# Kernel tuning notes

Measured on AMD Instinct MI355X. Metric: run time of the kernel, lower is better.

## Reference

```python
import jax, jax.numpy as jnp
import numpy as np

N_EMBD = 768
N_HEAD = 8
B, T = 4, 2048

def setup_inputs() -> dict:
    key = jax.random.key(0)
    k1, k2, k3, k4, k5 = jax.random.split(key, 5)
    C = N_EMBD
    s = 1.0 / np.sqrt(C)
    return {
        "x": jax.random.normal(k1, (B, T, C), dtype=jnp.float32),
        "W_attn": jax.random.normal(k2, (C, 3 * C), dtype=jnp.float32) * s,
        "b_attn": jnp.zeros((3 * C,), dtype=jnp.float32),
        "W_proj": jax.random.normal(k3, (C, C), dtype=jnp.float32) * s,
        "b_proj": jnp.zeros((C,), dtype=jnp.float32),
    }

def reference(x, W_attn, b_attn, W_proj, b_proj):
    Bs, Ts, C = x.shape
    H = N_HEAD
    hs = C // H
    qkv = x @ W_attn + b_attn                      # [B,T,3C]
    q, k, v = jnp.split(qkv, 3, axis=-1)
    # reshape to [B,H,T,hs]
    q = q.reshape(Bs, Ts, H, hs).transpose(0, 2, 1, 3)
    k = k.reshape(Bs, Ts, H, hs).transpose(0, 2, 1, 3)
    v = v.reshape(Bs, Ts, H, hs).transpose(0, 2, 1, 3)
    scale = 1.0 / jnp.sqrt(jnp.float32(hs))
    att = jnp.einsum('bhid,bhjd->bhij', q, k) * scale   # [B,H,T,T]
    mask = jnp.tril(jnp.ones((Ts, Ts), dtype=bool))
    att = jnp.where(mask, att, -jnp.inf)
    m = jnp.max(att, axis=-1, keepdims=True)
    e = jnp.where(mask, jnp.exp(att - m), 0.0)
    # original kernel divides by (sum + 1e-9)
    att = e / (jnp.sum(e, axis=-1, keepdims=True) + 1e-9)
    y = jnp.einsum('bhij,bhjd->bhid', att, v)           # [B,H,T,hs]
    y = y.transpose(0, 2, 1, 3).reshape(Bs, Ts, C)
    return y @ W_proj + b_proj
```

## Files before the change

kernel.cpp:

```cpp
#include <hip/hip_runtime.h>

typedef __bf16 bf16;
typedef __attribute__((ext_vector_type(4))) __bf16 bf16x4;
typedef __attribute__((ext_vector_type(8))) __bf16 bf16x8;
typedef __attribute__((ext_vector_type(4))) float f32x4;

#define B_   4
#define T_   2048
#define C_   768
#define H_   8
#define HS_  96
#define M_   (B_ * T_)
#define QKN_ (3 * C_)

#define NEG_BIG (-1e30f)

#define KSTR 104
#define VSTR 72
#define PSTR 72

__device__ __forceinline__ void gload_lds16(const bf16* g, bf16* l) {
    __builtin_amdgcn_global_load_lds(
        (const __attribute__((address_space(1))) uint32_t*)g,
        (__attribute__((address_space(3))) uint32_t*)l,
        16, 0, 0);
}

__global__ void transpose_kernel(const float* __restrict__ W, bf16* __restrict__ Wt,
                                 int R, int Cn) {
    __shared__ bf16 tile[32][33];
    int tx = threadIdx.x, ty = threadIdx.y;
    int x  = blockIdx.x * 32 + tx;
    int y0 = blockIdx.y * 32;
#pragma unroll
    for (int j = 0; j < 32; j += 8)
        tile[ty + j][tx] = (bf16)W[(size_t)(y0 + ty + j) * Cn + x];
    __syncthreads();
    int y2 = blockIdx.x * 32;
    int x2 = y0 + tx;
#pragma unroll
    for (int j = 0; j < 32; j += 8)
        Wt[(size_t)(y2 + ty + j) * R + x2] = tile[tx][ty + j];
}

__global__ void sentinel_kernel(float* __restrict__ out, int n) {
    int i = blockIdx.x * 256 + threadIdx.x;
    if (i < n) out[i] = 12345.0f;
}

__device__ __forceinline__ bf16x8 cvt8(f32x4 v0, f32x4 v1) {
    bf16x8 o;
#pragma unroll
    for (int i = 0; i < 4; ++i) { o[i] = (bf16)v0[i]; o[4 + i] = (bf16)v1[i]; }
    return o;
}

__global__ __launch_bounds__(256) void convert_bf16_kernel(const float* __restrict__ in,
                                                           bf16* __restrict__ out,
                                                           int n8) {
    int i = blockIdx.x * 256 + threadIdx.x;
    if (i >= n8) return;
    const float* p = in + (size_t)i * 8;
    f32x4 a = *(const f32x4*)p;
    f32x4 b = *(const f32x4*)(p + 4);
    *(bf16x8*)&out[(size_t)i * 8] = cvt8(a, b);
}

#define TILE_ELEMS (128 * 64)

__global__ __launch_bounds__(256) void gemm_qkv(const bf16* __restrict__ A,
                                                const bf16* __restrict__ Bt,
                                                const float* __restrict__ bias,
                                                bf16* __restrict__ Cmat,
                                                bf16* __restrict__ Vt,
                                                int M, int N, int K) {
    __shared__ bf16 lda[2 * TILE_ELEMS];
    __shared__ bf16 ldb[2 * TILE_ELEMS];
    int tid  = threadIdx.x;
    int w    = tid >> 6;
    int lane = tid & 63;
    int col  = lane & 15, quad = lane >> 4;
    int wr   = w >> 1, wc = w & 1;
    int m0   = blockIdx.y * 128, n0 = blockIdx.x * 128;

    int srow = lane >> 3;
    int scol = (lane & 7) * 8;
    const bf16* gA[4]; const bf16* gB[4]; bf16* lA[4]; bf16* lB[4];
#pragma unroll
    for (int i = 0; i < 4; ++i) {
        int seg = w * 4 + i;
        int row = seg * 8 + srow;
        gA[i] = &A[(size_t)(m0 + row) * K + scol];
        gB[i] = &Bt[(size_t)(n0 + row) * K + scol];
        lA[i] = &lda[seg * 512];
        lB[i] = &ldb[seg * 512];
    }

    const f32x4 zero = {0.f, 0.f, 0.f, 0.f};
    f32x4 acc[4][4];
#pragma unroll
    for (int mr = 0; mr < 4; ++mr)
#pragma unroll
        for (int nc = 0; nc < 4; ++nc) acc[mr][nc] = zero;

#pragma unroll
    for (int i = 0; i < 4; ++i) {
        gload_lds16(gA[i], lA[i]);
        gload_lds16(gB[i], lB[i]);
    }
    __syncthreads();

    int cur = 0;
    for (int k0 = 0; k0 < K; k0 += 64) {
        int nxt = cur ^ 1;
        if (k0 + 64 < K) {
#pragma unroll
            for (int i = 0; i < 4; ++i) {
                gload_lds16(gA[i] + k0 + 64, lA[i] + nxt * TILE_ELEMS);
                gload_lds16(gB[i] + k0 + 64, lB[i] + nxt * TILE_ELEMS);
            }
        }
        const bf16* la = &lda[cur * TILE_ELEMS];
        const bf16* lb = &ldb[cur * TILE_ELEMS];
#pragma unroll
        for (int ks = 0; ks < 2; ++ks) {
            bf16x8 af[4], bfr[4];
#pragma unroll
            for (int t = 0; t < 4; ++t) {
                af[t]  = *(const bf16x8*)&la[(wr * 64 + t * 16 + col) * 64 + ks * 32 + quad * 8];
                bfr[t] = *(const bf16x8*)&lb[(wc * 64 + t * 16 + col) * 64 + ks * 32 + quad * 8];
            }
#pragma unroll
            for (int mr = 0; mr < 4; ++mr)
#pragma unroll
                for (int nc = 0; nc < 4; ++nc)
                    acc[mr][nc] = __builtin_amdgcn_mfma_f32_16x16x32_bf16(
                        af[mr], bfr[nc], acc[mr][nc], 0, 0, 0);
        }
        __syncthreads();
        cur = nxt;
    }

#pragma unroll
    for (int nc = 0; nc < 4; ++nc) {
        int n = n0 + wc * 64 + nc * 16 + col;
        float bv = bias[n];
#pragma unroll
        for (int mr = 0; mr < 4; ++mr) {
#pragma unroll
            for (int r = 0; r < 4; ++r) {
                int row = m0 + wr * 64 + mr * 16 + quad * 4 + r;
                Cmat[(size_t)row * N + n] = (bf16)(acc[mr][nc][r] + bv);
            }
        }
    }
    if (n0 >= 2 * C_) {
        int batch = m0 >> 11;
        bf16* Vtb = Vt + (size_t)batch * C_ * T_;
        int t0 = (m0 & 2047) + wr * 64;
#pragma unroll
        for (int nc = 0; nc < 4; ++nc) {
            int n  = n0 + wc * 64 + nc * 16 + col;
            int vc = n - 2 * C_;
            float bv = bias[n];
#pragma unroll
            for (int mr = 0; mr < 4; ++mr) {
                int t = t0 + mr * 16 + quad * 4;
                bf16x4 pk = {(bf16)(acc[mr][nc][0] + bv), (bf16)(acc[mr][nc][1] + bv),
                             (bf16)(acc[mr][nc][2] + bv), (bf16)(acc[mr][nc][3] + bv)};
                *(bf16x4*)&Vtb[(size_t)vc * T_ + t] = pk;
            }
        }
    }
}

__global__ __launch_bounds__(256) void gemm_proj(const bf16* __restrict__ A,
                                                 const bf16* __restrict__ Bt,
                                                 const float* __restrict__ bias,
                                                 float* __restrict__ Cmat,
                                                 int M, int N, int K) {
    __shared__ bf16 lda[2 * TILE_ELEMS];
    __shared__ bf16 ldb[2 * TILE_ELEMS];
    int tid  = threadIdx.x;
    int w    = tid >> 6;
    int lane = tid & 63;
    int col  = lane & 15, quad = lane >> 4;
    int wr   = w >> 1, wc = w & 1;
    int m0   = blockIdx.y * 128, n0 = blockIdx.x * 128;

    int srow = lane >> 3;
    int scol = (lane & 7) * 8;
    const bf16* gA[4]; const bf16* gB[4]; bf16* lA[4]; bf16* lB[4];
#pragma unroll
    for (int i = 0; i < 4; ++i) {
        int seg = w * 4 + i;
        int row = seg * 8 + srow;
        gA[i] = &A[(size_t)(m0 + row) * K + scol];
        gB[i] = &Bt[(size_t)(n0 + row) * K + scol];
        lA[i] = &lda[seg * 512];
        lB[i] = &ldb[seg * 512];
    }

    const f32x4 zero = {0.f, 0.f, 0.f, 0.f};
    f32x4 acc[4][4];
#pragma unroll
    for (int mr = 0; mr < 4; ++mr)
#pragma unroll
        for (int nc = 0; nc < 4; ++nc) acc[mr][nc] = zero;

#pragma unroll
    for (int i = 0; i < 4; ++i) {
        gload_lds16(gA[i], lA[i]);
        gload_lds16(gB[i], lB[i]);
    }
    __syncthreads();

    int cur = 0;
    for (int k0 = 0; k0 < K; k0 += 64) {
        int nxt = cur ^ 1;
        if (k0 + 64 < K) {
#pragma unroll
            for (int i = 0; i < 4; ++i) {
                gload_lds16(gA[i] + k0 + 64, lA[i] + nxt * TILE_ELEMS);
                gload_lds16(gB[i] + k0 + 64, lB[i] + nxt * TILE_ELEMS);
            }
        }
        const bf16* la = &lda[cur * TILE_ELEMS];
        const bf16* lb = &ldb[cur * TILE_ELEMS];
#pragma unroll
        for (int ks = 0; ks < 2; ++ks) {
            bf16x8 af[4], bfr[4];
#pragma unroll
            for (int t = 0; t < 4; ++t) {
                af[t]  = *(const bf16x8*)&la[(wr * 64 + t * 16 + col) * 64 + ks * 32 + quad * 8];
                bfr[t] = *(const bf16x8*)&lb[(wc * 64 + t * 16 + col) * 64 + ks * 32 + quad * 8];
            }
#pragma unroll
            for (int mr = 0; mr < 4; ++mr)
#pragma unroll
                for (int nc = 0; nc < 4; ++nc)
                    acc[mr][nc] = __builtin_amdgcn_mfma_f32_16x16x32_bf16(
                        af[mr], bfr[nc], acc[mr][nc], 0, 0, 0);
        }
        __syncthreads();
        cur = nxt;
    }

#pragma unroll
    for (int nc = 0; nc < 4; ++nc) {
        int n = n0 + wc * 64 + nc * 16 + col;
        float bv = bias[n];
#pragma unroll
        for (int mr = 0; mr < 4; ++mr) {
#pragma unroll
            for (int r = 0; r < 4; ++r) {
                int row = m0 + wr * 64 + mr * 16 + quad * 4 + r;
                Cmat[(size_t)row * N + n] = acc[mr][nc][r] + bv;
            }
        }
    }
}

__global__ __launch_bounds__(256) void attn_kernel(const bf16* __restrict__ qkv,
                                                   const bf16* __restrict__ Vt,
                                                   bf16* __restrict__ y,
                                                   int nGroups) {
    __shared__ bf16 ldsK[64 * KSTR];
    __shared__ bf16 ldsV[96 * VSTR];
    __shared__ bf16 ldsP[4 * 16 * PSTR];
    const int bid  = blockIdx.x;
    const int qt   = 31 - bid / nGroups;
    const int g    = bid % nGroups;
    const int h    = g & 7, b = g >> 3;
    const int tid  = threadIdx.x;
    const int w    = tid >> 6, lane = tid & 63;
    const int col  = lane & 15, quad = lane >> 4;
    const float SCALE2 = 0.10206207261596577f * 1.4426950408889634f;
    const float M0 = 24.0f;
    const f32x4 zero = {0.f, 0.f, 0.f, 0.f};

    const bf16* qkvb = qkv + (size_t)b * T_ * QKN_;
    const bf16* Vtbh = Vt + (size_t)(b * H_ + h) * HS_ * T_;
    bf16* yb  = y + (size_t)b * T_ * C_;
    bf16* myP = &ldsP[w * 16 * PSTR];

    const int rbase = qt * 64 + w * 16;

    bf16x8 qf[3];
#pragma unroll
    for (int c = 0; c < 3; ++c)
        qf[c] = *(const bf16x8*)&qkvb[(size_t)(rbase + col) * QKN_ + h * HS_ + c * 32 + quad * 8];

    const bf16* pK[3]; const bf16* pV[3];
    bf16 *dK[3], *dV[3];
#pragma unroll
    for (int i = 0; i < 3; ++i) {
        int chunk = i * 256 + tid;
        int rK = chunk / 12, cK = chunk - rK * 12;
        pK[i] = qkvb + (size_t)rK * QKN_ + C_ + h * HS_ + cK * 8;
        dK[i] = &ldsK[rK * KSTR + cK * 8];
        int rV = chunk >> 3, cV = chunk & 7;
        pV[i] = Vtbh + (size_t)rV * T_ + cV * 8;
        dV[i] = &ldsV[rV * VSTR + cV * 8];
    }

    f32x4 o[6];
#pragma unroll
    for (int n2 = 0; n2 < 6; ++n2) o[n2] = zero;
    float lsum = 0.f;

    bf16x8 kreg[3], vreg[3];
#pragma unroll
    for (int i = 0; i < 3; ++i) {
        kreg[i] = *(const bf16x8*)pK[i];
        vreg[i] = *(const bf16x8*)pV[i];
        pK[i] += (size_t)64 * QKN_;
        pV[i] += 64;
    }

    const int njt = qt + 1;
    for (int jt = 0; jt < njt; ++jt) {
        int jb = jt * 64;
        __syncthreads();
#pragma unroll
        for (int i = 0; i < 3; ++i) {
            *(bf16x8*)dK[i] = kreg[i];
            *(bf16x8*)dV[i] = vreg[i];
        }
        __syncthreads();
        if (jt + 1 < njt) {
#pragma unroll
            for (int i = 0; i < 3; ++i) {
                kreg[i] = *(const bf16x8*)pK[i];
                vreg[i] = *(const bf16x8*)pV[i];
                pK[i] += (size_t)64 * QKN_;
                pV[i] += 64;
            }
        }

        bf16x8 kf[4][3];
#pragma unroll
        for (int nb = 0; nb < 4; ++nb)
#pragma unroll
            for (int c = 0; c < 3; ++c)
                kf[nb][c] = *(const bf16x8*)&ldsK[(nb * 16 + col) * KSTR + c * 32 + quad * 8];

        f32x4 st[4];
#pragma unroll
        for (int nb = 0; nb < 4; ++nb) st[nb] = zero;
#pragma unroll
        for (int c = 0; c < 3; ++c)
#pragma unroll
            for (int nb = 0; nb < 4; ++nb)
                st[nb] = __builtin_amdgcn_mfma_f32_16x16x32_bf16(
                    kf[nb][c], qf[c], st[nb], 0, 0, 0);

        if (jt == njt - 1) {
#pragma unroll
            for (int nb = 0; nb < 4; ++nb)
#pragma unroll
                for (int r = 0; r < 4; ++r) {
                    int jg = jb + nb * 16 + quad * 4 + r;
                    st[nb][r] = (jg <= rbase + col) ? fmaf(st[nb][r], SCALE2, -M0)
                                                    : NEG_BIG;
                }
        } else {
#pragma unroll
            for (int nb = 0; nb < 4; ++nb)
#pragma unroll
                for (int r = 0; r < 4; ++r)
                    st[nb][r] = fmaf(st[nb][r], SCALE2, -M0);
        }

#pragma unroll
        for (int nb = 0; nb < 4; ++nb) {
#pragma unroll
            for (int r = 0; r < 4; ++r) {
                float pv = exp2f(st[nb][r]);
                st[nb][r] = pv;
                lsum += pv;
            }
            bf16x4 pk = {(bf16)st[nb][0], (bf16)st[nb][1],
                         (bf16)st[nb][2], (bf16)st[nb][3]};
            *(bf16x4*)&myP[col * PSTR + nb * 16 + quad * 4] = pk;
        }

        bf16x8 vf[6][2];
#pragma unroll
        for (int n2 = 0; n2 < 6; ++n2)
#pragma unroll
            for (int c = 0; c < 2; ++c)
                vf[n2][c] = *(const bf16x8*)&ldsV[(n2 * 16 + col) * VSTR + c * 32 + quad * 8];
        bf16x8 pa0 = *(const bf16x8*)&myP[col * PSTR + quad * 8];
        bf16x8 pa1 = *(const bf16x8*)&myP[col * PSTR + 32 + quad * 8];
#pragma unroll
        for (int n2 = 0; n2 < 6; ++n2)
            o[n2] = __builtin_amdgcn_mfma_f32_16x16x32_bf16(vf[n2][0], pa0, o[n2], 0, 0, 0);
#pragma unroll
        for (int n2 = 0; n2 < 6; ++n2)
            o[n2] = __builtin_amdgcn_mfma_f32_16x16x32_bf16(vf[n2][1], pa1, o[n2], 0, 0, 0);
    }

    lsum += __shfl_xor(lsum, 16, 64);
    lsum += __shfl_xor(lsum, 32, 64);
    float linv = 1.0f / lsum;
#pragma unroll
    for (int n2 = 0; n2 < 6; ++n2) {
        bf16x4 pk = {(bf16)(o[n2][0] * linv), (bf16)(o[n2][1] * linv),
                     (bf16)(o[n2][2] * linv), (bf16)(o[n2][3] * linv)};
        *(bf16x4*)&yb[(size_t)(rbase + col) * C_ + h * HS_ + n2 * 16 + quad * 4] = pk;
    }
}

extern "C" void kernel_launch(void* const* d_in, const int* in_sizes, int n_in,
                              void* d_out, int out_size, void* d_ws, size_t ws_size,
                              hipStream_t stream) {
    (void)in_sizes; (void)n_in;
    const float* x      = (const float*)d_in[0];
    const float* W_attn = (const float*)d_in[1];
    const float* b_attn = (const float*)d_in[2];
    const float* W_proj = (const float*)d_in[3];
    const float* b_proj = (const float*)d_in[4];
    float* out = (float*)d_out;

    size_t e_wta = (size_t)QKN_ * C_;
    size_t e_wtp = (size_t)C_ * C_;
    size_t a_qkv = e_wta + e_wtp;
    size_t a_vt  = a_qkv + (size_t)M_ * QKN_;
    size_t a_yb  = a_vt + (size_t)M_ * C_;
    size_t needA = (a_yb + (size_t)M_ * C_) * sizeof(bf16);
    size_t b_qkv = e_wta + e_wtp;
    size_t b_vt  = b_qkv + (size_t)T_ * QKN_;
    size_t b_yb  = b_vt + (size_t)T_ * C_;
    size_t needB = (b_yb + (size_t)T_ * C_) * sizeof(bf16);

    if (ws_size >= needA) {
        bf16* Wt_attn = (bf16*)d_ws;
        bf16* Wt_proj = (bf16*)d_ws + e_wta;
        bf16* qkv     = (bf16*)d_ws + a_qkv;
        bf16* Vt      = (bf16*)d_ws + a_vt;
        bf16* yb      = (bf16*)d_ws + a_yb;
        bf16* xb      = yb;
        convert_bf16_kernel<<<dim3(M_ * C_ / 8 / 256), 256, 0, stream>>>(x, xb, M_ * C_ / 8);
        transpose_kernel<<<dim3(QKN_ / 32, C_ / 32), dim3(32, 8), 0, stream>>>(W_attn, Wt_attn, C_, QKN_);
        transpose_kernel<<<dim3(C_ / 32, C_ / 32), dim3(32, 8), 0, stream>>>(W_proj, Wt_proj, C_, C_);
        gemm_qkv<<<dim3(QKN_ / 128, M_ / 128), 256, 0, stream>>>(
            xb, Wt_attn, b_attn, qkv, Vt, M_, QKN_, C_);
        attn_kernel<<<dim3(32 * H_ * B_), 256, 0, stream>>>(qkv, Vt, yb, H_ * B_);
        gemm_proj<<<dim3(C_ / 128, M_ / 128), 256, 0, stream>>>(
            yb, Wt_proj, b_proj, out, M_, C_, C_);
    } else if (ws_size >= needB) {
        bf16* Wt_attn = (bf16*)d_ws;
        bf16* Wt_proj = (bf16*)d_ws + e_wta;
        bf16* qkv     = (bf16*)d_ws + b_qkv;
        bf16* Vt      = (bf16*)d_ws + b_vt;
        bf16* yb      = (bf16*)d_ws + b_yb;
        bf16* xb      = yb;
        transpose_kernel<<<dim3(QKN_ / 32, C_ / 32), dim3(32, 8), 0, stream>>>(W_attn, Wt_attn, C_, QKN_);
        transpose_kernel<<<dim3(C_ / 32, C_ / 32), dim3(32, 8), 0, stream>>>(W_proj, Wt_proj, C_, C_);
        for (int b = 0; b < B_; ++b) {
            const float* xf = x + (size_t)b * T_ * C_;
            float* outb     = out + (size_t)b * T_ * C_;
            convert_bf16_kernel<<<dim3(T_ * C_ / 8 / 256), 256, 0, stream>>>(xf, xb, T_ * C_ / 8);
            gemm_qkv<<<dim3(QKN_ / 128, T_ / 128), 256, 0, stream>>>(
                xb, Wt_attn, b_attn, qkv, Vt, T_, QKN_, C_);
            attn_kernel<<<dim3(32 * H_), 256, 0, stream>>>(qkv, Vt, yb, H_);
            gemm_proj<<<dim3(C_ / 128, T_ / 128), 256, 0, stream>>>(
                yb, Wt_proj, b_proj, outb, T_, C_, C_);
        }
    } else {
        sentinel_kernel<<<(out_size + 255) / 256, 256, 0, stream>>>(out, out_size);
    }
}
```

Measured before the change: 216.1 us.

## Keep attention probabilities in registers and merge prep kernels into one launch

The attention kernel no longer writes P to LDS and reads it back. It packs the exp'd scores straight into MFMA B-operands and permutes the V reads from LDS to match, using two 4-element loads per operand. This removes the LDS round trip and ldsP, and launch_bounds is raised to ask for higher occupancy. The input conversion and both weight transposes are merged into a single prep_kernel launch, which cuts launch overhead. The risk is that the register layout remap and the split bf16x4 V reads may cause more LDS bank conflicts or extra instructions.

```diff
diff --git a/kernel.cpp b/kernel.cpp
--- a/kernel.cpp
+++ b/kernel.cpp
@@ -17,13 +17,26 @@
 
 #define KSTR 104
 #define VSTR 72
-#define PSTR 72
 
 __device__ __forceinline__ void gload_lds16(const bf16* g, bf16* l) {
     __builtin_amdgcn_global_load_lds(
         (const __attribute__((address_space(1))) uint32_t*)g,
         (__attribute__((address_space(3))) uint32_t*)l,
         16, 0, 0);
+}
+
+__device__ __forceinline__ bf16x8 cvt8(f32x4 v0, f32x4 v1) {
+    bf16x8 o;
+#pragma unroll
+    for (int i = 0; i < 4; ++i) { o[i] = (bf16)v0[i]; o[4 + i] = (bf16)v1[i]; }
+    return o;
+}
+
+__device__ __forceinline__ bf16x8 cat4(bf16x4 a, bf16x4 b) {
+    bf16x8 o;
+#pragma unroll
+    for (int i = 0; i < 4; ++i) { o[i] = a[i]; o[4 + i] = b[i]; }
+    return o;
 }
 
 __global__ void transpose_kernel(const float* __restrict__ W, bf16* __restrict__ Wt,
@@ -46,13 +59,6 @@
 __global__ void sentinel_kernel(float* __restrict__ out, int n) {
     int i = blockIdx.x * 256 + threadIdx.x;
     if (i < n) out[i] = 12345.0f;
-}
-
-__device__ __forceinline__ bf16x8 cvt8(f32x4 v0, f32x4 v1) {
-    bf16x8 o;
-#pragma unroll
-    for (int i = 0; i < 4; ++i) { o[i] = (bf16)v0[i]; o[4 + i] = (bf16)v1[i]; }
-    return o;
 }
 
 __global__ __launch_bounds__(256) void convert_bf16_kernel(const float* __restrict__ in,
@@ -64,6 +70,54 @@
     f32x4 a = *(const f32x4*)p;
     f32x4 b = *(const f32x4*)(p + 4);
     *(bf16x8*)&out[(size_t)i * 8] = cvt8(a, b);
+}
+
+#define CONV_BLKS (M_ * C_ / 8 / 256)
+#define TA_BX (QKN_ / 32)
+#define TA_BLKS (TA_BX * (C_ / 32))
+#define TP_BX (C_ / 32)
+#define TP_BLKS (TP_BX * (C_ / 32))
+
+__device__ __forceinline__ void transpose_body(bf16 (*tile)[33],
+                                               const float* __restrict__ W,
+                                               bf16* __restrict__ Wt,
+                                               int R, int Cn, int bx, int by, int tid) {
+    int tx = tid & 31, ty = tid >> 5;
+    int x  = bx * 32 + tx;
+    int y0 = by * 32;
+#pragma unroll
+    for (int j = 0; j < 32; j += 8)
+        tile[ty + j][tx] = (bf16)W[(size_t)(y0 + ty + j) * Cn + x];
+    __syncthreads();
+    int y2 = bx * 32;
+    int x2 = y0 + tx;
+#pragma unroll
+    for (int j = 0; j < 32; j += 8)
+        Wt[(size_t)(y2 + ty + j) * R + x2] = tile[tx][ty + j];
+}
+
+__global__ __launch_bounds__(256) void prep_kernel(const float* __restrict__ x,
+                                                   bf16* __restrict__ xb,
+                                                   const float* __restrict__ Wa,
+                                                   bf16* __restrict__ Wta,
+                                                   const float* __restrict__ Wp,
+                                                   bf16* __restrict__ Wtp) {
+    __shared__ bf16 tile[32][33];
+    int bid = blockIdx.x;
+    int tid = threadIdx.x;
+    if (bid < CONV_BLKS) {
+        int i = bid * 256 + tid;
+        const float* p = x + (size_t)i * 8;
+        f32x4 a = *(const f32x4*)p;
+        f32x4 b = *(const f32x4*)(p + 4);
+        *(bf16x8*)&xb[(size_t)i * 8] = cvt8(a, b);
+    } else if (bid < CONV_BLKS + TA_BLKS) {
+        int t = bid - CONV_BLKS;
+        transpose_body(tile, Wa, Wta, C_, QKN_, t % TA_BX, t / TA_BX, tid);
+    } else {
+        int t = bid - CONV_BLKS - TA_BLKS;
+        transpose_body(tile, Wp, Wtp, C_, C_, t % TP_BX, t / TP_BX, tid);
+    }
 }
 
 #define TILE_ELEMS (128 * 64)
@@ -261,13 +315,12 @@
     }
 }
 
-__global__ __launch_bounds__(256) void attn_kernel(const bf16* __restrict__ qkv,
-                                                   const bf16* __restrict__ Vt,
-                                                   bf16* __restrict__ y,
-                                                   int nGroups) {
+__global__ __launch_bounds__(256, 6) void attn_kernel(const bf16* __restrict__ qkv,
+                                                      const bf16* __restrict__ Vt,
+                                                      bf16* __restrict__ y,
+                                                      int nGroups) {
     __shared__ bf16 ldsK[64 * KSTR];
     __shared__ bf16 ldsV[96 * VSTR];
-    __shared__ bf16 ldsP[4 * 16 * PSTR];
     const int bid  = blockIdx.x;
     const int qt   = 31 - bid / nGroups;
     const int g    = bid % nGroups;
@@ -282,7 +335,6 @@
     const bf16* qkvb = qkv + (size_t)b * T_ * QKN_;
     const bf16* Vtbh = Vt + (size_t)(b * H_ + h) * HS_ * T_;
     bf16* yb  = y + (size_t)b * T_ * C_;
-    bf16* myP = &ldsP[w * 16 * PSTR];
 
     const int rbase = qt * 64 + w * 16;
 
@@ -373,32 +425,33 @@
         }
 
 #pragma unroll
-        for (int nb = 0; nb < 4; ++nb) {
+        for (int nb = 0; nb < 4; ++nb)
 #pragma unroll
             for (int r = 0; r < 4; ++r) {
                 float pv = exp2f(st[nb][r]);
                 st[nb][r] = pv;
                 lsum += pv;
             }
-            bf16x4 pk = {(bf16)st[nb][0], (bf16)st[nb][1],
-                         (bf16)st[nb][2], (bf16)st[nb][3]};
-            *(bf16x4*)&myP[col * PSTR + nb * 16 + quad * 4] = pk;
-        }
-
-        bf16x8 vf[6][2];
-#pragma unroll
-        for (int n2 = 0; n2 < 6; ++n2)
-#pragma unroll
-            for (int c = 0; c < 2; ++c)
-                vf[n2][c] = *(const bf16x8*)&ldsV[(n2 * 16 + col) * VSTR + c * 32 + quad * 8];
-        bf16x8 pa0 = *(const bf16x8*)&myP[col * PSTR + quad * 8];
-        bf16x8 pa1 = *(const bf16x8*)&myP[col * PSTR + 32 + quad * 8];
-#pragma unroll
-        for (int n2 = 0; n2 < 6; ++n2)
-            o[n2] = __builtin_amdgcn_mfma_f32_16x16x32_bf16(vf[n2][0], pa0, o[n2], 0, 0, 0);
-#pragma unroll
-        for (int n2 = 0; n2 < 6; ++n2)
-            o[n2] = __builtin_amdgcn_mfma_f32_16x16x32_bf16(vf[n2][1], pa1, o[n2], 0, 0, 0);
+
+        bf16x8 palo, pahi;
+#pragma unroll
+        for (int r = 0; r < 4; ++r) {
+            palo[r]     = (bf16)st[0][r];
+            palo[4 + r] = (bf16)st[2][r];
+            pahi[r]     = (bf16)st[1][r];
+            pahi[4 + r] = (bf16)st[3][r];
+        }
+
+#pragma unroll
+        for (int n2 = 0; n2 < 6; ++n2) {
+            const bf16* vrow = &ldsV[(n2 * 16 + col) * VSTR];
+            bf16x8 vlo = cat4(*(const bf16x4*)&vrow[quad * 4],
+                              *(const bf16x4*)&vrow[32 + quad * 4]);
+            bf16x8 vhi = cat4(*(const bf16x4*)&vrow[16 + quad * 4],
+                              *(const bf16x4*)&vrow[48 + quad * 4]);
+            o[n2] = __builtin_amdgcn_mfma_f32_16x16x32_bf16(vlo, palo, o[n2], 0, 0, 0);
+            o[n2] = __builtin_amdgcn_mfma_f32_16x16x32_bf16(vhi, pahi, o[n2], 0, 0, 0);
+        }
     }
 
     lsum += __shfl_xor(lsum, 16, 64);
@@ -441,9 +494,8 @@
         bf16* Vt      = (bf16*)d_ws + a_vt;
         bf16* yb      = (bf16*)d_ws + a_yb;
         bf16* xb      = yb;
-        convert_bf16_kernel<<<dim3(M_ * C_ / 8 / 256), 256, 0, stream>>>(x, xb, M_ * C_ / 8);
-        transpose_kernel<<<dim3(QKN_ / 32, C_ / 32), dim3(32, 8), 0, stream>>>(W_attn, Wt_attn, C_, QKN_);
-        transpose_kernel<<<dim3(C_ / 32, C_ / 32), dim3(32, 8), 0, stream>>>(W_proj, Wt_proj, C_, C_);
+        prep_kernel<<<dim3(CONV_BLKS + TA_BLKS + TP_BLKS), 256, 0, stream>>>(
+            x, xb, W_attn, Wt_attn, W_proj, Wt_proj);
         gemm_qkv<<<dim3(QKN_ / 128, M_ / 128), 256, 0, stream>>>(
             xb, Wt_attn, b_attn, qkv, Vt, M_, QKN_, C_);
         attn_kernel<<<dim3(32 * H_ * B_), 256, 0, stream>>>(qkv, Vt, yb, H_ * B_);
```

Result: slower. 402.2 us (+86.1%).
